# Kernel tuning notes

Hardware: AMD Instinct MI355X
Metric: run time of the kernel (lower is better)

## Reference

```python
import jax, jax.numpy as jnp
import numpy as np

N_SEND = 12288   # 12 * 32^2
N_REC = 49152    # 12 * 64^2
E = 196608       # 4 * N_REC (knn with k=4)
D = 256
EIN, EOUT = 4, 256
LIN_IN, LIN_OUT = 512, 256
B = 2


def setup_inputs() -> dict:
    key = jax.random.key(0)
    ks = jax.random.split(key, 12)
    s = 0.05
    x = jax.random.normal(ks[0], (B, N_SEND, D), jnp.float32)
    edge_attr = jax.random.normal(ks[1], (E, EIN), jnp.float32)
    idx_send = jax.random.randint(ks[2], (E,), 0, N_SEND, dtype=jnp.int32)
    idx_rec = jnp.sort(jax.random.randint(ks[3], (E,), 0, N_REC, dtype=jnp.int32))
    return {
        "x": x,
        "edge_attr": edge_attr,
        "idx_send": idx_send,
        "idx_rec": idx_rec,
        "We1": jax.random.normal(ks[4], (EIN, EOUT), jnp.float32) * s,
        "be1": jnp.zeros((EOUT,), jnp.float32),
        "We2": jax.random.normal(ks[5], (EOUT, EOUT), jnp.float32) * s,
        "be2": jnp.zeros((EOUT,), jnp.float32),
        "Wl1": jax.random.normal(ks[6], (LIN_IN, LIN_OUT), jnp.float32) * s,
        "bl1": jnp.zeros((LIN_OUT,), jnp.float32),
        "Wl2": jax.random.normal(ks[7], (LIN_OUT, LIN_OUT), jnp.float32) * s,
        "bl2": jnp.zeros((LIN_OUT,), jnp.float32),
    }


def reference(x, edge_attr, idx_send, idx_rec, We1, be1, We2, be2, Wl1, bl1, Wl2, bl2):
    # edge embedder MLP: Linear -> GELU -> Linear   [E, EOUT]
    ef = jax.nn.gelu(edge_attr @ We1 + be1) @ We2 + be2
    # gather sender node features by edge           [B, E, D]
    v_s = x[:, idx_send, :]
    # concat gathered features with (batch-broadcast) edge embeddings [B, E, D+EOUT]
    ef_b = jnp.broadcast_to(ef[None], (v_s.shape[0],) + ef.shape)
    v_s_prime = jnp.concatenate([v_s, ef_b], axis=-1)
    # scatter_sum over receiver index along edge dim -> [B, N_REC, LIN_IN]
    agg = jax.vmap(lambda m: jax.ops.segment_sum(m, idx_rec, num_segments=N_REC))(v_s_prime)
    # final FeedForward: Linear -> GELU -> Linear
    return jax.nn.gelu(agg @ Wl1 + bl1) @ Wl2 + bl2
```

## Files before the change

kernel.cpp:

```cpp
#include <hip/hip_runtime.h>
#include <hip/hip_bf16.h>

#define N_SEND 12288
#define N_REC  49152
#define NEDGE  196608

typedef __attribute__((ext_vector_type(8)))  short short8;
typedef __attribute__((ext_vector_type(4)))  short shortx4;
typedef __attribute__((ext_vector_type(4)))  float floatx4;
typedef __attribute__((ext_vector_type(16))) float floatx16;
typedef __attribute__((ext_vector_type(4)))  unsigned int uintx4;

__device__ inline short f2bs(float f) {
    __hip_bfloat16 h = __float2bfloat16(f);
    return *reinterpret_cast<short*>(&h);
}
__device__ inline float gelu_tanh(float x) {
    const float k0 = 0.7978845608028654f;
    float u = k0 * (x + 0.044715f * x * x * x);
    float e = __expf(2.0f * u);
    float t = 1.0f - 2.0f / (e + 1.0f);
    return 0.5f * x * (1.0f + t);
}

__global__ void prep_kernel(const float* __restrict__ We2, const float* __restrict__ be2,
                            const float* __restrict__ Wl1, const float* __restrict__ Wl2,
                            short* __restrict__ BT1, short* __restrict__ WT2,
                            float* __restrict__ cvec) {
    int i = blockIdx.x;
    int n = threadIdx.x;
    if (i < 256) {
        float acc = 0.f;
        for (int j = 0; j < 256; ++j)
            acc += We2[i * 256 + j] * Wl1[(256 + j) * 256 + n];
        BT1[n * 512 + i]       = f2bs(Wl1[i * 256 + n]);
        BT1[n * 512 + 256 + i] = f2bs(acc);
        WT2[n * 256 + i]       = f2bs(Wl2[i * 256 + n]);
    } else {
        float acc = 0.f;
        for (int j = 0; j < 256; ++j)
            acc += be2[j] * Wl1[(256 + j) * 256 + n];
        cvec[n] = acc;
    }
}

__global__ void xcast_kernel(const float* __restrict__ X, short* __restrict__ Xb) {
    int i = (blockIdx.x * 256 + threadIdx.x) * 8;
    floatx4 v0 = *(const floatx4*)(X + i);
    floatx4 v1 = *(const floatx4*)(X + i + 4);
    short8 p;
#pragma unroll
    for (int j = 0; j < 4; ++j) { p[j] = f2bs(v0[j]); p[j + 4] = f2bs(v1[j]); }
    *(short8*)(Xb + i) = p;
}

__global__ void bounds_kernel(const int* __restrict__ idx_rec, int* __restrict__ bnd) {
    int r = blockIdx.x * 256 + threadIdx.x;
    if (r > N_REC) return;
    int lo = 0, hi = NEDGE;
    while (lo < hi) { int mid = (lo + hi) >> 1; if (idx_rec[mid] < r) lo = mid + 1; else hi = mid; }
    bnd[r] = lo;
}

#define XTU(f, row) ((((f) * 64) + ((row) ^ ((f) & 7))) * 8)
#define HTU(f, rl)  ((((f) * 32) + ((rl) ^ ((f) & 7))) * 8)

__global__ __launch_bounds__(512, 6)
void fused32(const int* __restrict__ idx_send, const int* __restrict__ bnd,
             const float* __restrict__ EA, const float* __restrict__ We1,
             const float* __restrict__ be1, const short* __restrict__ Xb,
             const short* __restrict__ BT1, const short* __restrict__ WT2,
             const float* __restrict__ cvec, const float* __restrict__ bl1,
             const float* __restrict__ bl2, float* __restrict__ OUT) {
    __shared__ __attribute__((aligned(16))) short XT[32 * 64 * 8];
    __shared__ __attribute__((aligned(16))) short HT[32 * 32 * 8];
    __shared__ int sb[33];

    int t = threadIdx.x;
    int r0 = blockIdx.x * 32;
    if (t <= 32) sb[t] = bnd[r0 + t];
    __syncthreads();

    {
        int cg = t & 31;
        int b  = (t >> 5) & 1;
        int rh = t >> 6;
        int c8 = cg * 8;
        int hc = c8 + 4 * b;

        floatx4 w0 = *(const floatx4*)(We1 + hc);
        floatx4 w1 = *(const floatx4*)(We1 + 256 + hc);
        floatx4 w2 = *(const floatx4*)(We1 + 512 + hc);
        floatx4 w3 = *(const floatx4*)(We1 + 768 + hc);
        floatx4 bb = *(const floatx4*)(be1 + hc);
        const short* xb_t = Xb + (size_t)b * N_SEND * 256 + c8;

#pragma unroll
        for (int r = 0; r < 4; ++r) {
            int rl = rh * 4 + r;
            int es = __builtin_amdgcn_readfirstlane(sb[rl]);
            int ee = __builtin_amdgcn_readfirstlane(sb[rl + 1]);

            float xacc[8];
            float hacc[4];
#pragma unroll
            for (int c = 0; c < 8; ++c) xacc[c] = 0.f;
#pragma unroll
            for (int c = 0; c < 4; ++c) hacc[c] = 0.f;

            for (int e = es; e < ee; ++e) {
                int s = idx_send[e];
                floatx4 a = *(const floatx4*)(EA + (size_t)e * 4);
                uintx4 xv = *(const uintx4*)(xb_t + (size_t)s * 256);
#pragma unroll
                for (int dw = 0; dw < 4; ++dw) {
                    xacc[2 * dw]     += __builtin_bit_cast(float, xv[dw] << 16);
                    xacc[2 * dw + 1] += __builtin_bit_cast(float, xv[dw] & 0xffff0000u);
                }
#pragma unroll
                for (int j = 0; j < 4; ++j) {
                    float u = a[0] * w0[j] + a[1] * w1[j] + a[2] * w2[j] + a[3] * w3[j] + bb[j];
                    hacc[j] += gelu_tanh(u);
                }
            }
            short8 xp;
#pragma unroll
            for (int c = 0; c < 8; ++c) xp[c] = f2bs(xacc[c]);
            *(short8*)(XT + XTU(cg, b * 32 + rl)) = xp;
            shortx4 hp;
#pragma unroll
            for (int c = 0; c < 4; ++c) hp[c] = f2bs(hacc[c]);
            *(shortx4*)(HT + HTU(cg, rl) + 4 * b) = hp;
        }
    }
    __syncthreads();

    int w = t >> 6, lane = t & 63;
    int m = lane & 31, q = lane >> 5;
    int wcol = w * 32;
    floatx16 acc0, acc1;
#pragma unroll
    for (int j = 0; j < 16; ++j) { acc0[j] = 0.f; acc1[j] = 0.f; }

    const short* Bp1 = BT1 + (size_t)(wcol + m) * 512 + q * 8;
#pragma unroll
    for (int ci = 0; ci < 8; ++ci) {
        short8 bf[4];
#pragma unroll
        for (int kk = 0; kk < 4; ++kk) bf[kk] = *(const short8*)(Bp1 + ci * 64 + kk * 16);
#pragma unroll
        for (int kk = 0; kk < 4; ++kk) {
            int f = ci * 8 + 2 * kk + q;
            short8 a0, a1;
            if (ci < 4) {
                a0 = *(const short8*)(XT + XTU(f, m));
                a1 = *(const short8*)(XT + XTU(f, 32 + m));
            } else {
                a0 = *(const short8*)(HT + HTU(f - 32, m));
                a1 = a0;
            }
            acc0 = __builtin_amdgcn_mfma_f32_32x32x16_bf16(bf[kk], a0, acc0, 0, 0, 0);
            acc1 = __builtin_amdgcn_mfma_f32_32x32x16_bf16(bf[kk], a1, acc1, 0, 0, 0);
        }
    }
    __syncthreads();

    {
        float cntv = (float)(sb[m + 1] - sb[m]);
#pragma unroll
        for (int qd = 0; qd < 4; ++qd) {
            int c0 = wcol + qd * 8 + q * 4;
            floatx4 cv  = *(const floatx4*)(cvec + c0);
            floatx4 b1v = *(const floatx4*)(bl1 + c0);
            shortx4 p0, p1;
#pragma unroll
            for (int j = 0; j < 4; ++j) {
                p0[j] = f2bs(gelu_tanh(acc0[qd * 4 + j] + cntv * cv[j] + b1v[j]));
                p1[j] = f2bs(gelu_tanh(acc1[qd * 4 + j] + cntv * cv[j] + b1v[j]));
            }
            *(shortx4*)(XT + XTU(w * 4 + qd, m)      + q * 4) = p0;
            *(shortx4*)(XT + XTU(w * 4 + qd, 32 + m) + q * 4) = p1;
        }
#pragma unroll
        for (int j = 0; j < 16; ++j) { acc0[j] = 0.f; acc1[j] = 0.f; }
    }
    __syncthreads();

    const short* Bp2 = WT2 + (size_t)(wcol + m) * 256 + q * 8;
#pragma unroll
    for (int ci = 0; ci < 4; ++ci) {
        short8 bf[4];
#pragma unroll
        for (int kk = 0; kk < 4; ++kk) bf[kk] = *(const short8*)(Bp2 + ci * 64 + kk * 16);
#pragma unroll
        for (int kk = 0; kk < 4; ++kk) {
            int f2 = ci * 8 + 2 * kk + q;
            short8 a0 = *(const short8*)(XT + XTU(f2, m));
            short8 a1 = *(const short8*)(XT + XTU(f2, 32 + m));
            acc0 = __builtin_amdgcn_mfma_f32_32x32x16_bf16(bf[kk], a0, acc0, 0, 0, 0);
            acc1 = __builtin_amdgcn_mfma_f32_32x32x16_bf16(bf[kk], a1, acc1, 0, 0, 0);
        }
    }

#pragma unroll
    for (int rt = 0; rt < 2; ++rt) {
        const floatx16& ac = rt ? acc1 : acc0;
        size_t obase = ((size_t)rt * N_REC + r0 + m) * 256;
#pragma unroll
        for (int qd = 0; qd < 4; ++qd) {
            int c0 = wcol + qd * 8 + q * 4;
            floatx4 bv = *(const floatx4*)(bl2 + c0);
            floatx4 o;
#pragma unroll
            for (int j = 0; j < 4; ++j)
                o[j] = ac[qd * 4 + j] + bv[j];
            *(floatx4*)(OUT + obase + c0) = o;
        }
    }
}

extern "C" void kernel_launch(void* const* d_in, const int* in_sizes, int n_in,
                              void* d_out, int out_size, void* d_ws, size_t ws_size,
                              hipStream_t stream) {
    const float* x        = (const float*)d_in[0];
    const float* ea       = (const float*)d_in[1];
    const int*   idx_send = (const int*)d_in[2];
    const int*   idx_rec  = (const int*)d_in[3];
    const float* We1      = (const float*)d_in[4];
    const float* be1      = (const float*)d_in[5];
    const float* We2      = (const float*)d_in[6];
    const float* be2      = (const float*)d_in[7];
    const float* Wl1      = (const float*)d_in[8];
    const float* bl1      = (const float*)d_in[9];
    const float* Wl2      = (const float*)d_in[10];
    const float* bl2      = (const float*)d_in[11];
    float* out = (float*)d_out;
    char*  ws  = (char*)d_ws;

    short* BT1  = (short*)(ws + 0);
    short* WT2  = (short*)(ws + 262144);
    float* cvec = (float*)(ws + 393216);
    int*   bnd  = (int*)  (ws + 397312);
    short* Xb   = (short*)(ws + 1048576);

    prep_kernel<<<257, 256, 0, stream>>>(We2, be2, Wl1, Wl2, BT1, WT2, cvec);
    xcast_kernel<<<(2 * N_SEND * 256) / (256 * 8), 256, 0, stream>>>(x, Xb);
    bounds_kernel<<<(N_REC + 1 + 255) / 256, 256, 0, stream>>>(idx_rec, bnd);
    fused32<<<N_REC / 32, 512, 0, stream>>>(idx_send, bnd, ea, We1, be1, Xb,
                                            BT1, WT2, cvec, bl1, bl2, out);
}
```

Before: 310.4 us.

## Grow fused block tile to 48 receivers and prefetch edge indices

Each block now handles 48 receivers instead of 32, so the two batches give 96 rows covered by three 32-row MFMA tiles. Weight B-fragments are reused across three tiles instead of two. The edge-embedding rows are remapped so the shared edge-feature block fills all tiles, and the ragged row tiles are mapped back to batch and receiver for the epilogue. The gather loop software-prefetches the next idx_send and edge_attr values to hide load latency. In exchange there is more LDS and register use and the occupancy hint drops from 6 to 4 blocks per CU.

```diff
diff --git a/kernel.cpp b/kernel.cpp
--- a/kernel.cpp
+++ b/kernel.cpp
@@ -4,6 +4,7 @@
 #define N_SEND 12288
 #define N_REC  49152
 #define NEDGE  196608
+#define RECV   48
 
 typedef __attribute__((ext_vector_type(8)))  short short8;
 typedef __attribute__((ext_vector_type(4)))  short shortx4;
@@ -62,23 +63,23 @@
     bnd[r] = lo;
 }
 
-#define XTU(f, row) ((((f) * 64) + ((row) ^ ((f) & 7))) * 8)
-#define HTU(f, rl)  ((((f) * 32) + ((rl) ^ ((f) & 7))) * 8)
-
-__global__ __launch_bounds__(512, 6)
-void fused32(const int* __restrict__ idx_send, const int* __restrict__ bnd,
+#define XTU(f, row) ((((f) * 96) + ((row) ^ ((f) & 7))) * 8)
+#define HTU(f, rl)  ((((f) * 48) + ((rl) ^ ((f) & 7))) * 8)
+
+__global__ __launch_bounds__(512, 4)
+void fused48(const int* __restrict__ idx_send, const int* __restrict__ bnd,
              const float* __restrict__ EA, const float* __restrict__ We1,
              const float* __restrict__ be1, const short* __restrict__ Xb,
              const short* __restrict__ BT1, const short* __restrict__ WT2,
              const float* __restrict__ cvec, const float* __restrict__ bl1,
              const float* __restrict__ bl2, float* __restrict__ OUT) {
-    __shared__ __attribute__((aligned(16))) short XT[32 * 64 * 8];
-    __shared__ __attribute__((aligned(16))) short HT[32 * 32 * 8];
-    __shared__ int sb[33];
+    __shared__ __attribute__((aligned(16))) short XT[32 * 96 * 8];
+    __shared__ __attribute__((aligned(16))) short HT[32 * 48 * 8];
+    __shared__ int sb[RECV + 1];
 
     int t = threadIdx.x;
-    int r0 = blockIdx.x * 32;
-    if (t <= 32) sb[t] = bnd[r0 + t];
+    int r0 = blockIdx.x * RECV;
+    if (t <= RECV) sb[t] = bnd[r0 + t];
     __syncthreads();
 
     {
@@ -96,8 +97,8 @@
         const short* xb_t = Xb + (size_t)b * N_SEND * 256 + c8;
 
 #pragma unroll
-        for (int r = 0; r < 4; ++r) {
-            int rl = rh * 4 + r;
+        for (int r = 0; r < 6; ++r) {
+            int rl = rh * 6 + r;
             int es = __builtin_amdgcn_readfirstlane(sb[rl]);
             int ee = __builtin_amdgcn_readfirstlane(sb[rl + 1]);
 
@@ -108,10 +109,14 @@
 #pragma unroll
             for (int c = 0; c < 4; ++c) hacc[c] = 0.f;
 
+            int s = 0; floatx4 a = {0.f, 0.f, 0.f, 0.f};
+            if (es < ee) { s = idx_send[es]; a = *(const floatx4*)(EA + (size_t)es * 4); }
             for (int e = es; e < ee; ++e) {
-                int s = idx_send[e];
-                floatx4 a = *(const floatx4*)(EA + (size_t)e * 4);
-                uintx4 xv = *(const uintx4*)(xb_t + (size_t)s * 256);
+                int cs = s; floatx4 ca = a;
+                int ep = (e + 1 < ee) ? e + 1 : e;
+                s = idx_send[ep];
+                a = *(const floatx4*)(EA + (size_t)ep * 4);
+                uintx4 xv = *(const uintx4*)(xb_t + (size_t)cs * 256);
 #pragma unroll
                 for (int dw = 0; dw < 4; ++dw) {
                     xacc[2 * dw]     += __builtin_bit_cast(float, xv[dw] << 16);
@@ -119,14 +124,14 @@
                 }
 #pragma unroll
                 for (int j = 0; j < 4; ++j) {
-                    float u = a[0] * w0[j] + a[1] * w1[j] + a[2] * w2[j] + a[3] * w3[j] + bb[j];
+                    float u = ca[0] * w0[j] + ca[1] * w1[j] + ca[2] * w2[j] + ca[3] * w3[j] + bb[j];
                     hacc[j] += gelu_tanh(u);
                 }
             }
             short8 xp;
 #pragma unroll
             for (int c = 0; c < 8; ++c) xp[c] = f2bs(xacc[c]);
-            *(short8*)(XT + XTU(cg, b * 32 + rl)) = xp;
+            *(short8*)(XT + XTU(cg, b * RECV + rl)) = xp;
             shortx4 hp;
 #pragma unroll
             for (int c = 0; c < 4; ++c) hp[c] = f2bs(hacc[c]);
@@ -138,74 +143,84 @@
     int w = t >> 6, lane = t & 63;
     int m = lane & 31, q = lane >> 5;
     int wcol = w * 32;
-    floatx16 acc0, acc1;
-#pragma unroll
-    for (int j = 0; j < 16; ++j) { acc0[j] = 0.f; acc1[j] = 0.f; }
+    floatx16 acc[3];
+#pragma unroll
+    for (int i = 0; i < 3; ++i)
+#pragma unroll
+        for (int j = 0; j < 16; ++j) acc[i][j] = 0.f;
 
     const short* Bp1 = BT1 + (size_t)(wcol + m) * 512 + q * 8;
 #pragma unroll
     for (int ci = 0; ci < 8; ++ci) {
-        short8 bf[4];
-#pragma unroll
-        for (int kk = 0; kk < 4; ++kk) bf[kk] = *(const short8*)(Bp1 + ci * 64 + kk * 16);
 #pragma unroll
         for (int kk = 0; kk < 4; ++kk) {
+            short8 bv = *(const short8*)(Bp1 + ci * 64 + kk * 16);
             int f = ci * 8 + 2 * kk + q;
-            short8 a0, a1;
+            short8 a0, a1, a2;
             if (ci < 4) {
                 a0 = *(const short8*)(XT + XTU(f, m));
                 a1 = *(const short8*)(XT + XTU(f, 32 + m));
+                a2 = *(const short8*)(XT + XTU(f, 64 + m));
             } else {
-                a0 = *(const short8*)(HT + HTU(f - 32, m));
-                a1 = a0;
+                int fh = f - 32;
+                a0 = *(const short8*)(HT + HTU(fh, m));
+                int rl1 = (m < 16) ? 32 + m : m - 16;
+                a1 = *(const short8*)(HT + HTU(fh, rl1));
+                a2 = *(const short8*)(HT + HTU(fh, 16 + m));
             }
-            acc0 = __builtin_amdgcn_mfma_f32_32x32x16_bf16(bf[kk], a0, acc0, 0, 0, 0);
-            acc1 = __builtin_amdgcn_mfma_f32_32x32x16_bf16(bf[kk], a1, acc1, 0, 0, 0);
-        }
-    }
-    __syncthreads();
-
-    {
-        float cntv = (float)(sb[m + 1] - sb[m]);
-#pragma unroll
-        for (int qd = 0; qd < 4; ++qd) {
-            int c0 = wcol + qd * 8 + q * 4;
-            floatx4 cv  = *(const floatx4*)(cvec + c0);
-            floatx4 b1v = *(const floatx4*)(bl1 + c0);
-            shortx4 p0, p1;
-#pragma unroll
-            for (int j = 0; j < 4; ++j) {
-                p0[j] = f2bs(gelu_tanh(acc0[qd * 4 + j] + cntv * cv[j] + b1v[j]));
-                p1[j] = f2bs(gelu_tanh(acc1[qd * 4 + j] + cntv * cv[j] + b1v[j]));
-            }
-            *(shortx4*)(XT + XTU(w * 4 + qd, m)      + q * 4) = p0;
-            *(shortx4*)(XT + XTU(w * 4 + qd, 32 + m) + q * 4) = p1;
-        }
-#pragma unroll
-        for (int j = 0; j < 16; ++j) { acc0[j] = 0.f; acc1[j] = 0.f; }
-    }
+            acc[0] = __builtin_amdgcn_mfma_f32_32x32x16_bf16(bv, a0, acc[0], 0, 0, 0);
+            acc[1] = __builtin_amdgcn_mfma_f32_32x32x16_bf16(bv, a1, acc[1], 0, 0, 0);
+            acc[2] = __builtin_amdgcn_mfma_f32_32x32x16_bf16(bv, a2, acc[2], 0, 0, 0);
+        }
+    }
+    __syncthreads();
+
+#pragma unroll
+    for (int qd = 0; qd < 4; ++qd) {
+        int c0 = wcol + qd * 8 + q * 4;
+        floatx4 cv  = *(const floatx4*)(cvec + c0);
+        floatx4 b1v = *(const floatx4*)(bl1 + c0);
+#pragma unroll
+        for (int rt = 0; rt < 3; ++rt) {
+            int r = rt * 32 + m;
+            int bat = (r >= RECV) ? 1 : 0;
+            int rl = r - RECV * bat;
+            float cntv = (float)(sb[rl + 1] - sb[rl]);
+            shortx4 pk;
+#pragma unroll
+            for (int j = 0; j < 4; ++j)
+                pk[j] = f2bs(gelu_tanh(acc[rt][qd * 4 + j] + cntv * cv[j] + b1v[j]));
+            *(shortx4*)(XT + XTU(w * 4 + qd, r) + q * 4) = pk;
+        }
+    }
+#pragma unroll
+    for (int i = 0; i < 3; ++i)
+#pragma unroll
+        for (int j = 0; j < 16; ++j) acc[i][j] = 0.f;
     __syncthreads();
 
     const short* Bp2 = WT2 + (size_t)(wcol + m) * 256 + q * 8;
 #pragma unroll
     for (int ci = 0; ci < 4; ++ci) {
-        short8 bf[4];
-#pragma unroll
-        for (int kk = 0; kk < 4; ++kk) bf[kk] = *(const short8*)(Bp2 + ci * 64 + kk * 16);
 #pragma unroll
         for (int kk = 0; kk < 4; ++kk) {
+            short8 bv = *(const short8*)(Bp2 + ci * 64 + kk * 16);
             int f2 = ci * 8 + 2 * kk + q;
             short8 a0 = *(const short8*)(XT + XTU(f2, m));
             short8 a1 = *(const short8*)(XT + XTU(f2, 32 + m));
-            acc0 = __builtin_amdgcn_mfma_f32_32x32x16_bf16(bf[kk], a0, acc0, 0, 0, 0);
-            acc1 = __builtin_amdgcn_mfma_f32_32x32x16_bf16(bf[kk], a1, acc1, 0, 0, 0);
-        }
-    }
-
-#pragma unroll
-    for (int rt = 0; rt < 2; ++rt) {
-        const floatx16& ac = rt ? acc1 : acc0;
-        size_t obase = ((size_t)rt * N_REC + r0 + m) * 256;
+            short8 a2 = *(const short8*)(XT + XTU(f2, 64 + m));
+            acc[0] = __builtin_amdgcn_mfma_f32_32x32x16_bf16(bv, a0, acc[0], 0, 0, 0);
+            acc[1] = __builtin_amdgcn_mfma_f32_32x32x16_bf16(bv, a1, acc[1], 0, 0, 0);
+            acc[2] = __builtin_amdgcn_mfma_f32_32x32x16_bf16(bv, a2, acc[2], 0, 0, 0);
+        }
+    }
+
+#pragma unroll
+    for (int rt = 0; rt < 3; ++rt) {
+        int r = rt * 32 + m;
+        int bat = (r >= RECV) ? 1 : 0;
+        int rl = r - RECV * bat;
+        size_t obase = ((size_t)bat * N_REC + r0 + rl) * 256;
 #pragma unroll
         for (int qd = 0; qd < 4; ++qd) {
             int c0 = wcol + qd * 8 + q * 4;
@@ -213,7 +228,7 @@
             floatx4 o;
 #pragma unroll
             for (int j = 0; j < 4; ++j)
-                o[j] = ac[qd * 4 + j] + bv[j];
+                o[j] = acc[rt][qd * 4 + j] + bv[j];
             *(floatx4*)(OUT + obase + c0) = o;
         }
     }
@@ -246,6 +261,6 @@
     prep_kernel<<<257, 256, 0, stream>>>(We2, be2, Wl1, Wl2, BT1, WT2, cvec);
     xcast_kernel<<<(2 * N_SEND * 256) / (256 * 8), 256, 0, stream>>>(x, Xb);
     bounds_kernel<<<(N_REC + 1 + 255) / 256, 256, 0, stream>>>(idx_rec, bnd);
-    fused32<<<N_REC / 32, 512, 0, stream>>>(idx_send, bnd, ea, We1, be1, Xb,
-                                            BT1, WT2, cvec, bl1, bl2, out);
-}
+    fused48<<<N_REC / RECV, 512, 0, stream>>>(idx_send, bnd, ea, We1, be1, Xb,
+                                              BT1, WT2, cvec, bl1, bl2, out);
+}
```

Result: faster. 280.5 us (-9.6%).
